# Kernel optimization log

Measured on AMD Instinct MI355X. Metric: run time of the kernel, lower is better.

The kernel has to match this reference:

```python
import jax, jax.numpy as jnp
import numpy as np

N = 100000          # nodes
E = 1600000         # edges
IN_F = 128          # in_features
OUT_F = 64          # attention_dim = out_features
H = 8               # heads
D_K = OUT_F // H    # 8


def setup_inputs() -> dict:
    key = jax.random.key(0)
    ks = jax.random.split(key, 8)
    x = jax.random.normal(ks[0], (N, IN_F), dtype=jnp.float32)
    edge = jax.random.randint(ks[1], (2, E), 0, N, dtype=jnp.int64)
    # Linear weights stored torch-style [out, in]; biases [out].
    Wq = jax.random.normal(ks[2], (OUT_F, IN_F), dtype=jnp.float32) * 0.02
    bq = jax.random.normal(ks[3], (OUT_F,), dtype=jnp.float32) * 0.02
    Wk = jax.random.normal(ks[4], (OUT_F, IN_F), dtype=jnp.float32) * 0.02
    bk = jax.random.normal(ks[5], (OUT_F,), dtype=jnp.float32) * 0.02
    Wv = jax.random.normal(ks[6], (OUT_F, IN_F), dtype=jnp.float32) * 0.02
    bv = jax.random.normal(ks[7], (OUT_F,), dtype=jnp.float32) * 0.02
    return {"x": x, "edge": edge, "Wq": Wq, "bq": bq, "Wk": Wk, "bk": bk, "Wv": Wv, "bv": bv}


def _segment_softmax(scores, seg_ids, num_segments):
    # scores: [E, H], seg_ids: [E]; stable softmax grouped by seg_ids
    seg_max = jax.ops.segment_max(scores, seg_ids, num_segments=num_segments)  # [N, H]
    seg_max = jnp.where(jnp.isfinite(seg_max), seg_max, 0.0)
    ex = jnp.exp(scores - seg_max[seg_ids])                                    # [E, H]
    denom = jax.ops.segment_sum(ex, seg_ids, num_segments=num_segments)        # [N, H]
    return ex / (denom[seg_ids] + 1e-16)


def reference(x, edge, Wq, bq, Wk, bk, Wv, bv):
    src_idx = edge[0]  # source node per edge (softmax group + output row)
    dst_idx = edge[1]  # destination node per edge (k/v gather)

    q = (x @ Wq.T + bq).reshape(N, H, D_K)  # [N, H, D_K]
    k = (x @ Wk.T + bk).reshape(N, H, D_K)
    v = (x @ Wv.T + bv).reshape(N, H, D_K)

    # per-edge dot-product attention scores over d_k
    prods = jnp.sum(q[src_idx] * k[dst_idx], axis=-1) / np.sqrt(D_K)  # [E, H]
    attn = _segment_softmax(prods, src_idx, N)                         # [E, H]

    # spmm per head, vectorized: out[i] = sum_{e: src=i} attn[e,h] * v[dst[e],h,:]
    msgs = attn[:, :, None] * v[dst_idx]                               # [E, H, D_K]
    out = jax.ops.segment_sum(msgs, src_idx, num_segments=N)           # [N, H, D_K]
    # head-major concat matches torch loop-concat of [N, D_K] blocks
    return out.reshape(N, H * D_K)
```

## Files before the change

### kernel.cpp

```cpp
#include <hip/hip_runtime.h>

#define N_NODES   100000
#define E_EDGES   1600000
#define IN_FEATS  128
#define OUT_FEATS 64
#define NH        8
#define DK        8

#define QKV_BLOCKS   782
#define CSTR         32
#define CAP          64

typedef __attribute__((ext_vector_type(8))) short short8;
typedef __attribute__((ext_vector_type(4))) float floatx4;

__device__ __forceinline__ ushort f2bf(float f) {
    uint u = __float_as_uint(f);
    u += 0x7FFF + ((u >> 16) & 1);
    return (ushort)(u >> 16);
}
__device__ __forceinline__ float bflo(uint u) { return __uint_as_float(u << 16); }
__device__ __forceinline__ float bfhi(uint u) { return __uint_as_float(u & 0xFFFF0000u); }

__global__ __launch_bounds__(256) void prep_kernel(
    const float* __restrict__ Wq, const float* __restrict__ Wk,
    const float* __restrict__ Wv, ushort* __restrict__ Wb)
{
    const int i = blockIdx.x * 256 + threadIdx.x;
    if (i >= 3072) return;
    const int m  = i >> 10;
    const int kc = (i >> 8) & 3;
    const int qd = (i >> 6) & 3;
    const int nt = (i >> 4) & 3;
    const int lm = i & 15;
    const float* W = (m == 0) ? Wq : (m == 1) ? Wk : Wv;
    const float* s = W + (16 * nt + lm) * IN_FEATS + 32 * kc + 8 * qd;
    const float4 f0 = ((const float4*)s)[0];
    const float4 f1 = ((const float4*)s)[1];
    ushort r[8];
    r[0] = f2bf(f0.x); r[1] = f2bf(f0.y); r[2] = f2bf(f0.z); r[3] = f2bf(f0.w);
    r[4] = f2bf(f1.x); r[5] = f2bf(f1.y); r[6] = f2bf(f1.z); r[7] = f2bf(f1.w);
    *(short8*)(Wb + (size_t)i * 8) = *(short8*)r;
}

__global__ __launch_bounds__(512) void qkv_hist_kernel(
    const float* __restrict__ x, const ushort* __restrict__ Wb,
    const float* __restrict__ bq, const float* __restrict__ bk,
    const float* __restrict__ bv,
    float* __restrict__ qo, uint* __restrict__ kvo,
    const int* __restrict__ src, const int* __restrict__ dst,
    int* __restrict__ cnt, int* __restrict__ csr)
{
    __shared__ short8 wlds[3072];

    if (blockIdx.x & 1) {
        const int i = (blockIdx.x >> 1) * 512 + threadIdx.x;
        if (i < E_EDGES / 4) {
            const int4 s4 = ((const int4*)src)[i];
            const int4 d4 = ((const int4*)dst)[i];
            const int px = atomicAdd(&cnt[s4.x * CSTR], 1);
            const int py = atomicAdd(&cnt[s4.y * CSTR], 1);
            const int pz = atomicAdd(&cnt[s4.z * CSTR], 1);
            const int pw = atomicAdd(&cnt[s4.w * CSTR], 1);
            if (px < CAP) csr[s4.x * CAP + px] = d4.x;
            if (py < CAP) csr[s4.y * CAP + py] = d4.y;
            if (pz < CAP) csr[s4.z * CAP + pz] = d4.z;
            if (pw < CAP) csr[s4.w * CAP + pw] = d4.w;
        }
        return;
    }

    const int t    = threadIdx.x;
    const int lane = t & 63;
    const int w    = t >> 6;
    const int lm   = lane & 15;
    const int qd   = lane >> 4;
    const int row0 = (blockIdx.x >> 1) * 128 + 16 * w;

    #pragma unroll
    for (int c = 0; c < 6; ++c) {
        const int i = t + 512 * c;
        wlds[i] = *(const short8*)(Wb + (size_t)i * 8);
    }

    const int  arow   = row0 + lm;
    const bool avalid = arow < N_NODES;
    short8 afrag[4];
    #pragma unroll
    for (int kc = 0; kc < 4; ++kc) {
        float4 f0 = make_float4(0.f, 0.f, 0.f, 0.f);
        float4 f1 = f0;
        if (avalid) {
            const float4* xp =
                (const float4*)(x + (size_t)arow * IN_FEATS + kc * 32 + qd * 8);
            f0 = xp[0];
            f1 = xp[1];
        }
        short8 a;
        a[0] = (short)f2bf(f0.x); a[1] = (short)f2bf(f0.y);
        a[2] = (short)f2bf(f0.z); a[3] = (short)f2bf(f0.w);
        a[4] = (short)f2bf(f1.x); a[5] = (short)f2bf(f1.y);
        a[6] = (short)f2bf(f1.z); a[7] = (short)f2bf(f1.w);
        afrag[kc] = a;
    }

    floatx4 qacc[4], kacc[4], vacc[4];
    #pragma unroll
    for (int nt = 0; nt < 4; ++nt) {
        const float bbq = bq[16 * nt + lm];
        const float bbk = bk[16 * nt + lm];
        const float bbv = bv[16 * nt + lm];
        qacc[nt] = (floatx4){bbq, bbq, bbq, bbq};
        kacc[nt] = (floatx4){bbk, bbk, bbk, bbk};
        vacc[nt] = (floatx4){bbv, bbv, bbv, bbv};
    }

    __syncthreads();

    #pragma unroll
    for (int kc = 0; kc < 4; ++kc) {
        const int fb = kc * 256 + qd * 64 + lm;
        #pragma unroll
        for (int nt = 0; nt < 4; ++nt) {
            const short8 bq8 = wlds[fb + nt * 16];
            const short8 bk8 = wlds[fb + nt * 16 + 1024];
            const short8 bv8 = wlds[fb + nt * 16 + 2048];
            qacc[nt] = __builtin_amdgcn_mfma_f32_16x16x32_bf16(afrag[kc], bq8, qacc[nt], 0, 0, 0);
            kacc[nt] = __builtin_amdgcn_mfma_f32_16x16x32_bf16(afrag[kc], bk8, kacc[nt], 0, 0, 0);
            vacc[nt] = __builtin_amdgcn_mfma_f32_16x16x32_bf16(afrag[kc], bv8, vacc[nt], 0, 0, 0);
        }
    }

    #pragma unroll
    for (int nt = 0; nt < 4; ++nt) {
        #pragma unroll
        for (int reg = 0; reg < 4; ++reg) {
            const int row = row0 + 4 * qd + reg;
            if (row < N_NODES) {
                qo[(size_t)row * OUT_FEATS + 16 * nt + lm] = qacc[nt][reg];
                const uint kb = f2bf(kacc[nt][reg]);
                const uint vb = f2bf(vacc[nt][reg]);
                kvo[(size_t)row * OUT_FEATS + 16 * nt + lm] = kb | (vb << 16);
            }
        }
    }
}

__global__ __launch_bounds__(256) void attn_kernel(
    const float* __restrict__ q, const uint* __restrict__ kv,
    const int* __restrict__ cnt, const int* __restrict__ csr,
    float* __restrict__ out)
{
    const int lane = threadIdx.x & 63;
    const int wv   = threadIdx.x >> 6;
    const int node = blockIdx.x * 4 + wv;
    const int h    = lane >> 3;
    const int jme  = lane & 7;

    const float4* qrow = (const float4*)(q + (size_t)node * OUT_FEATS + h * DK);
    const float4 qa = qrow[0];
    const float4 qb = qrow[1];

    int deg = cnt[node * CSTR];
    deg = deg < CAP ? deg : CAP;

    int dn_lane = 0;
    if (lane < deg) dn_lane = csr[node * CAP + lane];

    float den = 0.f;
    float a0 = 0.f, a1 = 0.f, a2 = 0.f, a3 = 0.f;
    float a4 = 0.f, a5 = 0.f, a6 = 0.f, a7 = 0.f;

    int g = 0;
    for (; g + 16 <= deg; g += 16) {
        const int dnA = __shfl(dn_lane, g + jme);
        const int dnB = __shfl(dn_lane, g + 8 + jme);
        const uint4* kpA = (const uint4*)(kv + (size_t)dnA * OUT_FEATS + h * DK);
        const uint4* kpB = (const uint4*)(kv + (size_t)dnB * OUT_FEATS + h * DK);
        const uint4 uaA = kpA[0];
        const uint4 ubA = kpA[1];
        const uint4 uaB = kpB[0];
        const uint4 ubB = kpB[1];

        float pA = qa.x * bflo(uaA.x) + qa.y * bflo(uaA.y) +
                   qa.z * bflo(uaA.z) + qa.w * bflo(uaA.w) +
                   qb.x * bflo(ubA.x) + qb.y * bflo(ubA.y) +
                   qb.z * bflo(ubA.z) + qb.w * bflo(ubA.w);
        float pB = qa.x * bflo(uaB.x) + qa.y * bflo(uaB.y) +
                   qa.z * bflo(uaB.z) + qa.w * bflo(uaB.w) +
                   qb.x * bflo(ubB.x) + qb.y * bflo(ubB.y) +
                   qb.z * bflo(ubB.z) + qb.w * bflo(ubB.w);
        const float exA = exp2f(pA * 0.51006971413f);
        const float exB = exp2f(pB * 0.51006971413f);

        den += exA;
        a0 += exA * bfhi(uaA.x); a1 += exA * bfhi(uaA.y);
        a2 += exA * bfhi(uaA.z); a3 += exA * bfhi(uaA.w);
        a4 += exA * bfhi(ubA.x); a5 += exA * bfhi(ubA.y);
        a6 += exA * bfhi(ubA.z); a7 += exA * bfhi(ubA.w);
        den += exB;
        a0 += exB * bfhi(uaB.x); a1 += exB * bfhi(uaB.y);
        a2 += exB * bfhi(uaB.z); a3 += exB * bfhi(uaB.w);
        a4 += exB * bfhi(ubB.x); a5 += exB * bfhi(ubB.y);
        a6 += exB * bfhi(ubB.z); a7 += exB * bfhi(ubB.w);
    }
    for (; g < deg; g += 8) {
        const int dn = __shfl(dn_lane, g + jme);
        const uint4* kvp = (const uint4*)(kv + (size_t)dn * OUT_FEATS + h * DK);
        const uint4 ua = kvp[0];
        const uint4 ub = kvp[1];

        float p = qa.x * bflo(ua.x) + qa.y * bflo(ua.y) +
                  qa.z * bflo(ua.z) + qa.w * bflo(ua.w) +
                  qb.x * bflo(ub.x) + qb.y * bflo(ub.y) +
                  qb.z * bflo(ub.z) + qb.w * bflo(ub.w);
        float ex = exp2f(p * 0.51006971413f);
        if (g + jme >= deg) ex = 0.f;

        den += ex;
        a0 += ex * bfhi(ua.x); a1 += ex * bfhi(ua.y);
        a2 += ex * bfhi(ua.z); a3 += ex * bfhi(ua.w);
        a4 += ex * bfhi(ub.x); a5 += ex * bfhi(ub.y);
        a6 += ex * bfhi(ub.z); a7 += ex * bfhi(ub.w);
    }

    #pragma unroll
    for (int m = 1; m <= 4; m <<= 1) {
        den += __shfl_xor(den, m);
        a0 += __shfl_xor(a0, m); a1 += __shfl_xor(a1, m);
        a2 += __shfl_xor(a2, m); a3 += __shfl_xor(a3, m);
        a4 += __shfl_xor(a4, m); a5 += __shfl_xor(a5, m);
        a6 += __shfl_xor(a6, m); a7 += __shfl_xor(a7, m);
    }

    float r = a0;
    r = (jme == 1) ? a1 : r;
    r = (jme == 2) ? a2 : r;
    r = (jme == 3) ? a3 : r;
    r = (jme == 4) ? a4 : r;
    r = (jme == 5) ? a5 : r;
    r = (jme == 6) ? a6 : r;
    r = (jme == 7) ? a7 : r;

    out[(size_t)node * OUT_FEATS + lane] = r / (den + 1e-16f);
}

extern "C" void kernel_launch(void* const* d_in, const int* in_sizes, int n_in,
                              void* d_out, int out_size, void* d_ws, size_t ws_size,
                              hipStream_t stream)
{
    const float* x  = (const float*)d_in[0];
    const int*  edge = (const int*)d_in[1];
    const float* Wq = (const float*)d_in[2];
    const float* bq = (const float*)d_in[3];
    const float* Wk = (const float*)d_in[4];
    const float* bk = (const float*)d_in[5];
    const float* Wv = (const float*)d_in[6];
    const float* bv = (const float*)d_in[7];
    float* out = (float*)d_out;

    float* q  = (float*)d_ws;
    uint*  kv = (uint*)(q + (size_t)N_NODES * OUT_FEATS);
    int* cnt   = (int*)(kv + (size_t)N_NODES * OUT_FEATS);
    ushort* Wb = (ushort*)(cnt + (size_t)N_NODES * CSTR);
    int* csr   = (int*)(Wb + 3 * 64 * IN_FEATS);

    const int* src = edge;
    const int* dst = edge + E_EDGES;

    hipMemsetAsync(cnt, 0, (size_t)N_NODES * CSTR * sizeof(int), stream);

    prep_kernel<<<12, 256, 0, stream>>>(Wq, Wk, Wv, Wb);

    qkv_hist_kernel<<<QKV_BLOCKS * 2, 512, 0, stream>>>(
        x, Wb, bq, bk, bv, q, kv, src, dst, cnt, csr);

    attn_kernel<<<N_NODES / 4, 256, 0, stream>>>(q, kv, cnt, csr, out);
}
```

Before: 258.9 us.

## Interleave edge histogram with QKV MFMA in same threads; fold memset into prep

Zeroing of the per-node count array moves from a separate hipMemsetAsync into the weight-prep kernel, which is enlarged to cover the count buffer. The QKV kernel no longer dedicates odd blocks to the edge histogram. Instead every thread loads its edge indices early, issues the atomics after the LDS barrier, and writes the CSR entries after the MFMA stores, so atomic latency overlaps the matrix work. This halves the grid and removes one launch, but raises per-thread register pressure and ties histogram progress to GEMM block scheduling.

```diff
diff --git a/kernel.cpp b/kernel.cpp
--- a/kernel.cpp
+++ b/kernel.cpp
@@ -10,6 +10,8 @@
 #define QKV_BLOCKS   782
 #define CSTR         32
 #define CAP          64
+#define E4           (E_EDGES / 4)
+#define CNT4         (N_NODES * CSTR / 4)
 
 typedef __attribute__((ext_vector_type(8))) short short8;
 typedef __attribute__((ext_vector_type(4))) float floatx4;
@@ -24,23 +26,26 @@
 
 __global__ __launch_bounds__(256) void prep_kernel(
     const float* __restrict__ Wq, const float* __restrict__ Wk,
-    const float* __restrict__ Wv, ushort* __restrict__ Wb)
+    const float* __restrict__ Wv, ushort* __restrict__ Wb,
+    int* __restrict__ cnt)
 {
     const int i = blockIdx.x * 256 + threadIdx.x;
-    if (i >= 3072) return;
-    const int m  = i >> 10;
-    const int kc = (i >> 8) & 3;
-    const int qd = (i >> 6) & 3;
-    const int nt = (i >> 4) & 3;
-    const int lm = i & 15;
-    const float* W = (m == 0) ? Wq : (m == 1) ? Wk : Wv;
-    const float* s = W + (16 * nt + lm) * IN_FEATS + 32 * kc + 8 * qd;
-    const float4 f0 = ((const float4*)s)[0];
-    const float4 f1 = ((const float4*)s)[1];
-    ushort r[8];
-    r[0] = f2bf(f0.x); r[1] = f2bf(f0.y); r[2] = f2bf(f0.z); r[3] = f2bf(f0.w);
-    r[4] = f2bf(f1.x); r[5] = f2bf(f1.y); r[6] = f2bf(f1.z); r[7] = f2bf(f1.w);
-    *(short8*)(Wb + (size_t)i * 8) = *(short8*)r;
+    if (i < CNT4) ((int4*)cnt)[i] = make_int4(0, 0, 0, 0);
+    if (i < 3072) {
+        const int m  = i >> 10;
+        const int kc = (i >> 8) & 3;
+        const int qd = (i >> 6) & 3;
+        const int nt = (i >> 4) & 3;
+        const int lm = i & 15;
+        const float* W = (m == 0) ? Wq : (m == 1) ? Wk : Wv;
+        const float* s = W + (16 * nt + lm) * IN_FEATS + 32 * kc + 8 * qd;
+        const float4 f0 = ((const float4*)s)[0];
+        const float4 f1 = ((const float4*)s)[1];
+        ushort r[8];
+        r[0] = f2bf(f0.x); r[1] = f2bf(f0.y); r[2] = f2bf(f0.z); r[3] = f2bf(f0.w);
+        r[4] = f2bf(f1.x); r[5] = f2bf(f1.y); r[6] = f2bf(f1.z); r[7] = f2bf(f1.w);
+        *(short8*)(Wb + (size_t)i * 8) = *(short8*)r;
+    }
 }
 
 __global__ __launch_bounds__(512) void qkv_hist_kernel(
@@ -53,29 +58,20 @@
 {
     __shared__ short8 wlds[3072];
 
-    if (blockIdx.x & 1) {
-        const int i = (blockIdx.x >> 1) * 512 + threadIdx.x;
-        if (i < E_EDGES / 4) {
-            const int4 s4 = ((const int4*)src)[i];
-            const int4 d4 = ((const int4*)dst)[i];
-            const int px = atomicAdd(&cnt[s4.x * CSTR], 1);
-            const int py = atomicAdd(&cnt[s4.y * CSTR], 1);
-            const int pz = atomicAdd(&cnt[s4.z * CSTR], 1);
-            const int pw = atomicAdd(&cnt[s4.w * CSTR], 1);
-            if (px < CAP) csr[s4.x * CAP + px] = d4.x;
-            if (py < CAP) csr[s4.y * CAP + py] = d4.y;
-            if (pz < CAP) csr[s4.z * CAP + pz] = d4.z;
-            if (pw < CAP) csr[s4.w * CAP + pw] = d4.w;
-        }
-        return;
-    }
-
     const int t    = threadIdx.x;
     const int lane = t & 63;
     const int w    = t >> 6;
     const int lm   = lane & 15;
     const int qd   = lane >> 4;
-    const int row0 = (blockIdx.x >> 1) * 128 + 16 * w;
+    const int row0 = blockIdx.x * 128 + 16 * w;
+
+    const int  ei   = blockIdx.x * 512 + t;
+    const bool eval = ei < E4;
+    int4 s4 = make_int4(0, 0, 0, 0), d4 = make_int4(0, 0, 0, 0);
+    if (eval) {
+        s4 = ((const int4*)src)[ei];
+        d4 = ((const int4*)dst)[ei];
+    }
 
     #pragma unroll
     for (int c = 0; c < 6; ++c) {
@@ -117,6 +113,14 @@
 
     __syncthreads();
 
+    int px = 0, py = 0, pz = 0, pw = 0;
+    if (eval) {
+        px = atomicAdd(&cnt[s4.x * CSTR], 1);
+        py = atomicAdd(&cnt[s4.y * CSTR], 1);
+        pz = atomicAdd(&cnt[s4.z * CSTR], 1);
+        pw = atomicAdd(&cnt[s4.w * CSTR], 1);
+    }
+
     #pragma unroll
     for (int kc = 0; kc < 4; ++kc) {
         const int fb = kc * 256 + qd * 64 + lm;
@@ -144,6 +148,13 @@
             }
         }
     }
+
+    if (eval) {
+        if (px < CAP) csr[s4.x * CAP + px] = d4.x;
+        if (py < CAP) csr[s4.y * CAP + py] = d4.y;
+        if (pz < CAP) csr[s4.z * CAP + pz] = d4.z;
+        if (pw < CAP) csr[s4.w * CAP + pw] = d4.w;
+    }
 }
 
 __global__ __launch_bounds__(256) void attn_kernel(
@@ -268,11 +279,9 @@
     const int* src = edge;
     const int* dst = edge + E_EDGES;
 
-    hipMemsetAsync(cnt, 0, (size_t)N_NODES * CSTR * sizeof(int), stream);
-
-    prep_kernel<<<12, 256, 0, stream>>>(Wq, Wk, Wv, Wb);
-
-    qkv_hist_kernel<<<QKV_BLOCKS * 2, 512, 0, stream>>>(
+    prep_kernel<<<(CNT4 + 255) / 256, 256, 0, stream>>>(Wq, Wk, Wv, Wb, cnt);
+
+    qkv_hist_kernel<<<QKV_BLOCKS, 512, 0, stream>>>(
         x, Wb, bq, bk, bv, q, kv, src, dst, cnt, csr);
 
     attn_kernel<<<N_NODES / 4, 256, 0, stream>>>(q, kv, cnt, csr, out);
```

After: 278.7 us. 1.08x slower.

## Split QKV projection across separate blocks per matrix and fold counter zeroing into prep

Applied to the files above, without the earlier changes.

The fused QKV block now computes only one of Q, K or V per block (four block types per tile, the fourth doing the edge histogram), which cuts the LDS weight footprint to a third and lowers register pressure. K and V are written as interleaved 16-bit halves via separate short stores instead of one packed 32-bit store. The hipMemsetAsync of the counter array is replaced by zeroing inside the enlarged prep kernel, removing one launch. The trade-off is that each tile's x rows are now loaded and converted three times, and the K/V writes become narrower, strided stores.

```diff
diff --git a/kernel.cpp b/kernel.cpp
--- a/kernel.cpp
+++ b/kernel.cpp
@@ -7,9 +7,12 @@
 #define NH        8
 #define DK        8
 
-#define QKV_BLOCKS   782
+#define TILES        782
+#define TOTAL_BLOCKS (TILES * 4)
 #define CSTR         32
 #define CAP          64
+#define E4           (E_EDGES / 4)
+#define CNT4         (N_NODES * CSTR / 4)
 
 typedef __attribute__((ext_vector_type(8))) short short8;
 typedef __attribute__((ext_vector_type(4))) float floatx4;
@@ -24,38 +27,44 @@
 
 __global__ __launch_bounds__(256) void prep_kernel(
     const float* __restrict__ Wq, const float* __restrict__ Wk,
-    const float* __restrict__ Wv, ushort* __restrict__ Wb)
+    const float* __restrict__ Wv, ushort* __restrict__ Wb,
+    int* __restrict__ cnt)
 {
     const int i = blockIdx.x * 256 + threadIdx.x;
-    if (i >= 3072) return;
-    const int m  = i >> 10;
-    const int kc = (i >> 8) & 3;
-    const int qd = (i >> 6) & 3;
-    const int nt = (i >> 4) & 3;
-    const int lm = i & 15;
-    const float* W = (m == 0) ? Wq : (m == 1) ? Wk : Wv;
-    const float* s = W + (16 * nt + lm) * IN_FEATS + 32 * kc + 8 * qd;
-    const float4 f0 = ((const float4*)s)[0];
-    const float4 f1 = ((const float4*)s)[1];
-    ushort r[8];
-    r[0] = f2bf(f0.x); r[1] = f2bf(f0.y); r[2] = f2bf(f0.z); r[3] = f2bf(f0.w);
-    r[4] = f2bf(f1.x); r[5] = f2bf(f1.y); r[6] = f2bf(f1.z); r[7] = f2bf(f1.w);
-    *(short8*)(Wb + (size_t)i * 8) = *(short8*)r;
+    if (i < CNT4) ((int4*)cnt)[i] = make_int4(0, 0, 0, 0);
+    if (i < 3072) {
+        const int m  = i >> 10;
+        const int kc = (i >> 8) & 3;
+        const int qd = (i >> 6) & 3;
+        const int nt = (i >> 4) & 3;
+        const int lm = i & 15;
+        const float* W = (m == 0) ? Wq : (m == 1) ? Wk : Wv;
+        const float* s = W + (16 * nt + lm) * IN_FEATS + 32 * kc + 8 * qd;
+        const float4 f0 = ((const float4*)s)[0];
+        const float4 f1 = ((const float4*)s)[1];
+        ushort r[8];
+        r[0] = f2bf(f0.x); r[1] = f2bf(f0.y); r[2] = f2bf(f0.z); r[3] = f2bf(f0.w);
+        r[4] = f2bf(f1.x); r[5] = f2bf(f1.y); r[6] = f2bf(f1.z); r[7] = f2bf(f1.w);
+        *(short8*)(Wb + (size_t)i * 8) = *(short8*)r;
+    }
 }
 
 __global__ __launch_bounds__(512) void qkv_hist_kernel(
     const float* __restrict__ x, const ushort* __restrict__ Wb,
     const float* __restrict__ bq, const float* __restrict__ bk,
     const float* __restrict__ bv,
-    float* __restrict__ qo, uint* __restrict__ kvo,
+    float* __restrict__ qo, ushort* __restrict__ kvs,
     const int* __restrict__ src, const int* __restrict__ dst,
     int* __restrict__ cnt, int* __restrict__ csr)
 {
-    __shared__ short8 wlds[3072];
-
-    if (blockIdx.x & 1) {
-        const int i = (blockIdx.x >> 1) * 512 + threadIdx.x;
-        if (i < E_EDGES / 4) {
+    __shared__ short8 wlds[1024];
+
+    const int b = blockIdx.x;
+    const int t = threadIdx.x;
+
+    if ((b & 3) == 3) {
+        const int i = (b >> 2) * 512 + t;
+        if (i < E4) {
             const int4 s4 = ((const int4*)src)[i];
             const int4 d4 = ((const int4*)dst)[i];
             const int px = atomicAdd(&cnt[s4.x * CSTR], 1);
@@ -70,17 +79,18 @@
         return;
     }
 
-    const int t    = threadIdx.x;
+    const int m    = b & 3;
+    const int tile = b >> 2;
     const int lane = t & 63;
     const int w    = t >> 6;
     const int lm   = lane & 15;
     const int qd   = lane >> 4;
-    const int row0 = (blockIdx.x >> 1) * 128 + 16 * w;
-
-    #pragma unroll
-    for (int c = 0; c < 6; ++c) {
+    const int row0 = tile * 128 + 16 * w;
+
+    #pragma unroll
+    for (int c = 0; c < 2; ++c) {
         const int i = t + 512 * c;
-        wlds[i] = *(const short8*)(Wb + (size_t)i * 8);
+        wlds[i] = *(const short8*)(Wb + (size_t)(m * 1024 + i) * 8);
     }
 
     const int  arow   = row0 + lm;
@@ -104,15 +114,12 @@
         afrag[kc] = a;
     }
 
-    floatx4 qacc[4], kacc[4], vacc[4];
+    const float* bias = (m == 0) ? bq : (m == 1) ? bk : bv;
+    floatx4 acc[4];
     #pragma unroll
     for (int nt = 0; nt < 4; ++nt) {
-        const float bbq = bq[16 * nt + lm];
-        const float bbk = bk[16 * nt + lm];
-        const float bbv = bv[16 * nt + lm];
-        qacc[nt] = (floatx4){bbq, bbq, bbq, bbq};
-        kacc[nt] = (floatx4){bbk, bbk, bbk, bbk};
-        vacc[nt] = (floatx4){bbv, bbv, bbv, bbv};
+        const float bb = bias[16 * nt + lm];
+        acc[nt] = (floatx4){bb, bb, bb, bb};
     }
 
     __syncthreads();
@@ -122,25 +129,31 @@
         const int fb = kc * 256 + qd * 64 + lm;
         #pragma unroll
         for (int nt = 0; nt < 4; ++nt) {
-            const short8 bq8 = wlds[fb + nt * 16];
-            const short8 bk8 = wlds[fb + nt * 16 + 1024];
-            const short8 bv8 = wlds[fb + nt * 16 + 2048];
-            qacc[nt] = __builtin_amdgcn_mfma_f32_16x16x32_bf16(afrag[kc], bq8, qacc[nt], 0, 0, 0);
-            kacc[nt] = __builtin_amdgcn_mfma_f32_16x16x32_bf16(afrag[kc], bk8, kacc[nt], 0, 0, 0);
-            vacc[nt] = __builtin_amdgcn_mfma_f32_16x16x32_bf16(afrag[kc], bv8, vacc[nt], 0, 0, 0);
-        }
-    }
-
-    #pragma unroll
-    for (int nt = 0; nt < 4; ++nt) {
+            const short8 b8 = wlds[fb + nt * 16];
+            acc[nt] = __builtin_amdgcn_mfma_f32_16x16x32_bf16(afrag[kc], b8, acc[nt], 0, 0, 0);
+        }
+    }
+
+    if (m == 0) {
         #pragma unroll
-        for (int reg = 0; reg < 4; ++reg) {
-            const int row = row0 + 4 * qd + reg;
-            if (row < N_NODES) {
-                qo[(size_t)row * OUT_FEATS + 16 * nt + lm] = qacc[nt][reg];
-                const uint kb = f2bf(kacc[nt][reg]);
-                const uint vb = f2bf(vacc[nt][reg]);
-                kvo[(size_t)row * OUT_FEATS + 16 * nt + lm] = kb | (vb << 16);
+        for (int nt = 0; nt < 4; ++nt) {
+            #pragma unroll
+            for (int reg = 0; reg < 4; ++reg) {
+                const int row = row0 + 4 * qd + reg;
+                if (row < N_NODES)
+                    qo[(size_t)row * OUT_FEATS + 16 * nt + lm] = acc[nt][reg];
+            }
+        }
+    } else {
+        const int off = m - 1;
+        #pragma unroll
+        for (int nt = 0; nt < 4; ++nt) {
+            #pragma unroll
+            for (int reg = 0; reg < 4; ++reg) {
+                const int row = row0 + 4 * qd + reg;
+                if (row < N_NODES)
+                    kvs[((size_t)row * OUT_FEATS + 16 * nt + lm) * 2 + off] =
+                        f2bf(acc[nt][reg]);
             }
         }
     }
@@ -268,12 +281,10 @@
     const int* src = edge;
     const int* dst = edge + E_EDGES;
 
-    hipMemsetAsync(cnt, 0, (size_t)N_NODES * CSTR * sizeof(int), stream);
-
-    prep_kernel<<<12, 256, 0, stream>>>(Wq, Wk, Wv, Wb);
-
-    qkv_hist_kernel<<<QKV_BLOCKS * 2, 512, 0, stream>>>(
-        x, Wb, bq, bk, bv, q, kv, src, dst, cnt, csr);
+    prep_kernel<<<(CNT4 + 255) / 256, 256, 0, stream>>>(Wq, Wk, Wv, Wb, cnt);
+
+    qkv_hist_kernel<<<TOTAL_BLOCKS, 512, 0, stream>>>(
+        x, Wb, bq, bk, bv, q, (ushort*)kv, src, dst, cnt, csr);
 
     attn_kernel<<<N_NODES / 4, 256, 0, stream>>>(q, kv, cnt, csr, out);
 }
```

Result: slower. 310.0 us (+19.7%).

## Halve weight LDS footprint with two-phase staging and fuse count zeroing into prep

Applied to the files above, without the earlier changes.

The weight tile in shared memory drops from 48KB to 24KB by staging the K dimension in two halves, with syncs between phases. This lets more 512-thread blocks (including the histogram blocks) co-reside per CU. The Wb layout in prep_kernel is reordered to match. The separate hipMemsetAsync of the count array is replaced by zeroing inside prep_kernel, launched with enough blocks to cover it. The cost is extra barriers and a second global-to-LDS load in the GEMM blocks.

```diff
diff --git a/kernel.cpp b/kernel.cpp
--- a/kernel.cpp
+++ b/kernel.cpp
@@ -10,6 +10,8 @@
 #define QKV_BLOCKS   782
 #define CSTR         32
 #define CAP          64
+#define E4           (E_EDGES / 4)
+#define CNT4         (N_NODES * CSTR / 4)
 
 typedef __attribute__((ext_vector_type(8))) short short8;
 typedef __attribute__((ext_vector_type(4))) float floatx4;
@@ -24,23 +26,27 @@
 
 __global__ __launch_bounds__(256) void prep_kernel(
     const float* __restrict__ Wq, const float* __restrict__ Wk,
-    const float* __restrict__ Wv, ushort* __restrict__ Wb)
+    const float* __restrict__ Wv, ushort* __restrict__ Wb,
+    int* __restrict__ cnt)
 {
     const int i = blockIdx.x * 256 + threadIdx.x;
-    if (i >= 3072) return;
-    const int m  = i >> 10;
-    const int kc = (i >> 8) & 3;
-    const int qd = (i >> 6) & 3;
-    const int nt = (i >> 4) & 3;
-    const int lm = i & 15;
-    const float* W = (m == 0) ? Wq : (m == 1) ? Wk : Wv;
-    const float* s = W + (16 * nt + lm) * IN_FEATS + 32 * kc + 8 * qd;
-    const float4 f0 = ((const float4*)s)[0];
-    const float4 f1 = ((const float4*)s)[1];
-    ushort r[8];
-    r[0] = f2bf(f0.x); r[1] = f2bf(f0.y); r[2] = f2bf(f0.z); r[3] = f2bf(f0.w);
-    r[4] = f2bf(f1.x); r[5] = f2bf(f1.y); r[6] = f2bf(f1.z); r[7] = f2bf(f1.w);
-    *(short8*)(Wb + (size_t)i * 8) = *(short8*)r;
+    if (i < CNT4) ((int4*)cnt)[i] = make_int4(0, 0, 0, 0);
+    if (i < 3072) {
+        const int m  = i >> 10;
+        const int kc = (i >> 8) & 3;
+        const int qd = (i >> 6) & 3;
+        const int nt = (i >> 4) & 3;
+        const int lm = i & 15;
+        const float* W = (m == 0) ? Wq : (m == 1) ? Wk : Wv;
+        const float* s = W + (16 * nt + lm) * IN_FEATS + 32 * kc + 8 * qd;
+        const float4 f0 = ((const float4*)s)[0];
+        const float4 f1 = ((const float4*)s)[1];
+        ushort r[8];
+        r[0] = f2bf(f0.x); r[1] = f2bf(f0.y); r[2] = f2bf(f0.z); r[3] = f2bf(f0.w);
+        r[4] = f2bf(f1.x); r[5] = f2bf(f1.y); r[6] = f2bf(f1.z); r[7] = f2bf(f1.w);
+        const int di = (kc >> 1) * 1536 + m * 512 + (kc & 1) * 256 + qd * 64 + nt * 16 + lm;
+        *(short8*)(Wb + (size_t)di * 8) = *(short8*)r;
+    }
 }
 
 __global__ __launch_bounds__(512) void qkv_hist_kernel(
@@ -51,11 +57,11 @@
     const int* __restrict__ src, const int* __restrict__ dst,
     int* __restrict__ cnt, int* __restrict__ csr)
 {
-    __shared__ short8 wlds[3072];
+    __shared__ short8 wlds[1536];
 
     if (blockIdx.x & 1) {
         const int i = (blockIdx.x >> 1) * 512 + threadIdx.x;
-        if (i < E_EDGES / 4) {
+        if (i < E4) {
             const int4 s4 = ((const int4*)src)[i];
             const int4 d4 = ((const int4*)dst)[i];
             const int px = atomicAdd(&cnt[s4.x * CSTR], 1);
@@ -78,7 +84,7 @@
     const int row0 = (blockIdx.x >> 1) * 128 + 16 * w;
 
     #pragma unroll
-    for (int c = 0; c < 6; ++c) {
+    for (int c = 0; c < 3; ++c) {
         const int i = t + 512 * c;
         wlds[i] = *(const short8*)(Wb + (size_t)i * 8);
     }
@@ -118,13 +124,37 @@
     __syncthreads();
 
     #pragma unroll
-    for (int kc = 0; kc < 4; ++kc) {
-        const int fb = kc * 256 + qd * 64 + lm;
+    for (int kc = 0; kc < 2; ++kc) {
+        const int fb = (kc & 1) * 256 + qd * 64 + lm;
         #pragma unroll
         for (int nt = 0; nt < 4; ++nt) {
             const short8 bq8 = wlds[fb + nt * 16];
-            const short8 bk8 = wlds[fb + nt * 16 + 1024];
-            const short8 bv8 = wlds[fb + nt * 16 + 2048];
+            const short8 bk8 = wlds[fb + nt * 16 + 512];
+            const short8 bv8 = wlds[fb + nt * 16 + 1024];
+            qacc[nt] = __builtin_amdgcn_mfma_f32_16x16x32_bf16(afrag[kc], bq8, qacc[nt], 0, 0, 0);
+            kacc[nt] = __builtin_amdgcn_mfma_f32_16x16x32_bf16(afrag[kc], bk8, kacc[nt], 0, 0, 0);
+            vacc[nt] = __builtin_amdgcn_mfma_f32_16x16x32_bf16(afrag[kc], bv8, vacc[nt], 0, 0, 0);
+        }
+    }
+
+    __syncthreads();
+
+    #pragma unroll
+    for (int c = 0; c < 3; ++c) {
+        const int i = t + 512 * c;
+        wlds[i] = *(const short8*)(Wb + (size_t)(1536 + i) * 8);
+    }
+
+    __syncthreads();
+
+    #pragma unroll
+    for (int kc = 2; kc < 4; ++kc) {
+        const int fb = (kc & 1) * 256 + qd * 64 + lm;
+        #pragma unroll
+        for (int nt = 0; nt < 4; ++nt) {
+            const short8 bq8 = wlds[fb + nt * 16];
+            const short8 bk8 = wlds[fb + nt * 16 + 512];
+            const short8 bv8 = wlds[fb + nt * 16 + 1024];
             qacc[nt] = __builtin_amdgcn_mfma_f32_16x16x32_bf16(afrag[kc], bq8, qacc[nt], 0, 0, 0);
             kacc[nt] = __builtin_amdgcn_mfma_f32_16x16x32_bf16(afrag[kc], bk8, kacc[nt], 0, 0, 0);
             vacc[nt] = __builtin_amdgcn_mfma_f32_16x16x32_bf16(afrag[kc], bv8, vacc[nt], 0, 0, 0);
@@ -268,9 +298,7 @@
     const int* src = edge;
     const int* dst = edge + E_EDGES;
 
-    hipMemsetAsync(cnt, 0, (size_t)N_NODES * CSTR * sizeof(int), stream);
-
-    prep_kernel<<<12, 256, 0, stream>>>(Wq, Wk, Wv, Wb);
+    prep_kernel<<<(CNT4 + 255) / 256, 256, 0, stream>>>(Wq, Wk, Wv, Wb, cnt);
 
     qkv_hist_kernel<<<QKV_BLOCKS * 2, 512, 0, stream>>>(
         x, Wb, bq, bk, bv, q, kv, src, dst, cnt, csr);
```

New measurement: 258.3 us. About the same (-0.2%).
